# Kernel tuning notes

Measured on AMD Instinct MI355X. Metric: run time of the kernel, lower is better.

## Reference

```python
import jax, jax.numpy as jnp
import numpy as np

BETA = 0.95      # leak
THRESH = 1.0     # snntorch Leaky default threshold
ALPHA = 2.0      # ATan surrogate alpha (atan_with_alpha)
T = 100          # SPIKE_STEPS
D_IN = 65536     # input_dims
HID = 256        # fc1 hidden (hardcoded)
N_OUT = 20       # n_actions(2) * NUM_NEURONS_PER_ACTION(10)


def spike_fn(x):
    # forward of snntorch surrogate.ATan: Heaviside
    return (x > 0.0).astype(x.dtype)


def lif_step(mem, cur):
    # snntorch Leaky, reset_mechanism='subtract':
    # reset computed from previous membrane (detached), then decay+integrate, then fire
    reset = jax.lax.stop_gradient((mem > THRESH).astype(mem.dtype))
    mem_new = BETA * mem + cur - reset * THRESH
    spk = spike_fn(mem_new - THRESH)
    return spk, mem_new


def _run_net(x, W1, b1, W2, b2):
    # x: [T, D_IN]. Precompute all layer-1 currents as one big GEMM, then scan the recurrence.
    cur1_all = x @ W1.T + b1  # [T, HID]

    def step(carry, cur1):
        mem1, mem2 = carry
        spk1, mem1 = lif_step(mem1, cur1)
        cur2 = spk1 @ W2.T + b2  # [n_out]
        spk2, mem2 = lif_step(mem2, cur2)
        return (mem1, mem2), spk2

    init = (jnp.zeros((W1.shape[0],), x.dtype), jnp.zeros((W2.shape[0],), x.dtype))
    (_, mem2_final), spk2_hist = jax.lax.scan(step, init, cur1_all)
    return spk2_hist, mem2_final  # [T, n_out], [n_out]


def setup_inputs() -> dict:
    key = jax.random.key(0)
    ks = jax.random.split(key, 5)
    s = 0.01
    return {
        "poisson_spikes": jax.random.uniform(ks[0], (T, 1, D_IN), dtype=jnp.float32),
        "aW1": jax.random.normal(ks[1], (HID, D_IN), dtype=jnp.float32) * s,
        "ab1": jnp.zeros((HID,), jnp.float32),
        "aW2": jax.random.normal(ks[2], (N_OUT, HID), dtype=jnp.float32) * s,
        "ab2": jnp.zeros((N_OUT,), jnp.float32),
        "cW1": jax.random.normal(ks[3], (HID, D_IN), dtype=jnp.float32) * s,
        "cb1": jnp.zeros((HID,), jnp.float32),
        "cW2": jax.random.normal(ks[4], (1, HID), dtype=jnp.float32) * s,
        "cb2": jnp.zeros((1,), jnp.float32),
    }


def reference(poisson_spikes, aW1, ab1, aW2, ab2, cW1, cb1, cW2, cb2):
    x = poisson_spikes[:, 0, :]  # effective batch of 1 -> [T, D_IN]
    actor_spk_hist, _ = _run_net(x, aW1, ab1, aW2, ab2)        # [T, 20]
    _, critic_mem = _run_net(x, cW1, cb1, cW2, cb2)            # [1]
    spk_sum = actor_spk_hist.sum(axis=0)                       # [20] (sum over timesteps)
    action_vals = jnp.stack([spk_sum[:10].sum(), spk_sum[10:].sum()])
    policy = jax.nn.softmax(action_vals)                       # [2]
    return policy, critic_mem
```

## Files before the change

### kernel.cpp

```cpp
#include <hip/hip_runtime.h>
#include <hip/hip_bf16.h>

#define T_STEPS 100
#define D_IN    65536
#define HID     256
#define HTOT    512
#define BETA    0.95f
#define THRESH  1.0f

typedef __bf16 bf16x8 __attribute__((ext_vector_type(8)));
typedef float  f32x16 __attribute__((ext_vector_type(16)));

__device__ __forceinline__ void gload_lds16(const void* g, void* l) {
    __builtin_amdgcn_global_load_lds(
        (const __attribute__((address_space(1))) void*)g,
        (__attribute__((address_space(3))) void*)l, 16, 0, 0);
}

__global__ __launch_bounds__(256, 2) void k_gemm1(
    const float* __restrict__ aW1,
    const float* __restrict__ cW1,
    const float* __restrict__ x,
    float* __restrict__ P,
    int nsteps)
{
    const int d    = blockIdx.x;
    const int xcd  = d & 7;
    const int sl   = d >> 3;
    const int s    = xcd * 16 + (sl & 15);
    const int ht   = sl >> 4;

    const int tid  = threadIdx.x;
    const int lane = tid & 63;
    const int l31  = lane & 31;
    const int h5   = lane >> 5;
    const int wv   = tid >> 6;
    const int wt   = (wv & 1) * 64;
    const int wh   = (wv >> 1) * 64;

    __shared__ __align__(16) char smem[2][32768];

    const float* Wbase = (ht < 2) ? (aW1 + (size_t)ht * 128 * D_IN)
                                  : (cW1 + (size_t)(ht - 2) * 128 * D_IN);

    const float* xsrc[4];
    const float* wsrc[4];
#pragma unroll
    for (int o = 0; o < 4; o++) {
        const int idx = o * 256 + tid;
        const int row = idx >> 3, g = idx & 7;
        const int xrow = (row < T_STEPS) ? row : (T_STEPS - 1);
        xsrc[o] = x     + (size_t)xrow * D_IN + (g ^ (row & 7)) * 4;
        wsrc[o] = Wbase + (size_t)row  * D_IN + (g ^ (row & 7)) * 4;
    }
    const int gk0 = s * nsteps;

    f32x16 acc00, acc01, acc10, acc11;
#pragma unroll
    for (int i = 0; i < 16; i++) {
        acc00[i] = 0.f; acc01[i] = 0.f; acc10[i] = 0.f; acc11[i] = 0.f;
    }

#define STAGE(i) do {                                                         \
    char* b_ = smem[(i) & 1];                                                 \
    const int kc_ = (gk0 + (i)) * 32;                                         \
    _Pragma("unroll")                                                         \
    for (int o = 0; o < 4; o++) {                                             \
        const int g_ = o * 256 + tid;                                         \
        gload_lds16(xsrc[o] + kc_, b_ + g_ * 16);                             \
    }                                                                         \
    _Pragma("unroll")                                                         \
    for (int o = 0; o < 4; o++) {                                             \
        const int g_ = o * 256 + tid;                                         \
        gload_lds16(wsrc[o] + kc_, b_ + 16384 + g_ * 16);                     \
    }                                                                         \
} while (0)

#define CVT8(dsth, dstm, va, vb) do {                                         \
    float f_[8] = {va.x, va.y, va.z, va.w, vb.x, vb.y, vb.z, vb.w};           \
    _Pragma("unroll")                                                         \
    for (int e = 0; e < 8; e++) {                                             \
        __bf16 h = (__bf16)f_[e];                                             \
        dsth[e] = h; dstm[e] = (__bf16)(f_[e] - (float)h);                    \
    }                                                                         \
} while (0)

#define COMPUTE(i) do {                                                       \
    const char* b_ = smem[(i) & 1];                                           \
    _Pragma("unroll")                                                         \
    for (int s16 = 0; s16 < 2; s16++) {                                       \
        const int slot_ = s16 * 2 + h5;                                       \
        const int gb    = slot_ * 2;                                          \
            \
        const int r0 = wt + l31, r1 = r0 + 32;                                \
        const char* xr0_ = b_ + r0 * 128;                                     \
        const char* xr1_ = b_ + r1 * 128;                                     \
        float4 xa0 = *(const float4*)(xr0_ + ((gb ^ (r0 & 7)) * 16));         \
        float4 xb0 = *(const float4*)(xr0_ + (((gb + 1) ^ (r0 & 7)) * 16));   \
        float4 xa1 = *(const float4*)(xr1_ + ((gb ^ (r1 & 7)) * 16));         \
        float4 xb1 = *(const float4*)(xr1_ + (((gb + 1) ^ (r1 & 7)) * 16));   \
        bf16x8 a0h, a0m, a1h, a1m;                                            \
        CVT8(a0h, a0m, xa0, xb0);                                             \
        CVT8(a1h, a1m, xa1, xb1);                                             \
                      \
        const int hrA = wh + l31, hrB = hrA + 32;                             \
        const char* wrA_ = b_ + 16384 + hrA * 128;                            \
        const char* wrB_ = b_ + 16384 + hrB * 128;                            \
        float4 waA = *(const float4*)(wrA_ + ((gb ^ (hrA & 7)) * 16));        \
        float4 wbA = *(const float4*)(wrA_ + (((gb + 1) ^ (hrA & 7)) * 16));  \
        float4 waB = *(const float4*)(wrB_ + ((gb ^ (hrB & 7)) * 16));        \
        float4 wbB = *(const float4*)(wrB_ + (((gb + 1) ^ (hrB & 7)) * 16));  \
        bf16x8 bhA, bmA, bhB, bmB;                                            \
        CVT8(bhA, bmA, waA, wbA);                                             \
        CVT8(bhB, bmB, waB, wbB);                                             \
        acc00 = __builtin_amdgcn_mfma_f32_32x32x16_bf16(a0m, bhA, acc00, 0,0,0); \
        acc00 = __builtin_amdgcn_mfma_f32_32x32x16_bf16(a0h, bmA, acc00, 0,0,0); \
        acc00 = __builtin_amdgcn_mfma_f32_32x32x16_bf16(a0h, bhA, acc00, 0,0,0); \
        acc01 = __builtin_amdgcn_mfma_f32_32x32x16_bf16(a0m, bhB, acc01, 0,0,0); \
        acc01 = __builtin_amdgcn_mfma_f32_32x32x16_bf16(a0h, bmB, acc01, 0,0,0); \
        acc01 = __builtin_amdgcn_mfma_f32_32x32x16_bf16(a0h, bhB, acc01, 0,0,0); \
        acc10 = __builtin_amdgcn_mfma_f32_32x32x16_bf16(a1m, bhA, acc10, 0,0,0); \
        acc10 = __builtin_amdgcn_mfma_f32_32x32x16_bf16(a1h, bmA, acc10, 0,0,0); \
        acc10 = __builtin_amdgcn_mfma_f32_32x32x16_bf16(a1h, bhA, acc10, 0,0,0); \
        acc11 = __builtin_amdgcn_mfma_f32_32x32x16_bf16(a1m, bhB, acc11, 0,0,0); \
        acc11 = __builtin_amdgcn_mfma_f32_32x32x16_bf16(a1h, bmB, acc11, 0,0,0); \
        acc11 = __builtin_amdgcn_mfma_f32_32x32x16_bf16(a1h, bhB, acc11, 0,0,0); \
    }                                                                         \
} while (0)

    STAGE(0);
    STAGE(1);
    for (int i = 0; i < nsteps; i++) {
        if (i + 1 < nsteps) asm volatile("s_waitcnt vmcnt(8)" ::: "memory");
        else                asm volatile("s_waitcnt vmcnt(0)" ::: "memory");
        __builtin_amdgcn_s_barrier();
        __builtin_amdgcn_sched_barrier(0);
        COMPUTE(i);
        __builtin_amdgcn_s_barrier();
        __builtin_amdgcn_sched_barrier(0);
        if (i + 2 < nsteps) STAGE(i + 2);
    }
#undef STAGE
#undef CVT8
#undef COMPUTE

    const int rbase = 4 * h5;
    float* Pb = P + (size_t)s * T_STEPS * HTOT;
    const int hA = ht * 128 + wh + l31;
    const int hB = hA + 32;
#pragma unroll
    for (int reg = 0; reg < 16; reg++) {
        const int row = (reg & 3) + rbase + 8 * (reg >> 2);
        const int t0  = wt + row;
        const int t1  = wt + 32 + row;
        if (t0 < T_STEPS) {
            Pb[(size_t)t0 * HTOT + hA] = acc00[reg];
            Pb[(size_t)t0 * HTOT + hB] = acc01[reg];
        }
        if (t1 < T_STEPS) {
            Pb[(size_t)t1 * HTOT + hA] = acc10[reg];
            Pb[(size_t)t1 * HTOT + hB] = acc11[reg];
        }
    }
}

__global__ __launch_bounds__(256) void k_reduce(
    const float* __restrict__ P,
    const float* __restrict__ ab1, const float* __restrict__ cb1,
    float* __restrict__ cur1, int NS)
{
    int g4 = blockIdx.x * 256 + threadIdx.x;
    int g  = g4 * 4;
    int h0 = g & (HTOT - 1);
    float4 sum;
    sum.x = (h0 + 0 < HID) ? ab1[h0 + 0] : cb1[h0 + 0 - HID];
    sum.y = (h0 + 1 < HID) ? ab1[h0 + 1] : cb1[h0 + 1 - HID];
    sum.z = (h0 + 2 < HID) ? ab1[h0 + 2] : cb1[h0 + 2 - HID];
    sum.w = (h0 + 3 < HID) ? ab1[h0 + 3] : cb1[h0 + 3 - HID];
    for (int ss = 0; ss < NS; ss++) {
        float4 v = *(const float4*)(P + (size_t)ss * T_STEPS * HTOT + g);
        sum.x += v.x; sum.y += v.y; sum.z += v.z; sum.w += v.w;
    }
    *(float4*)(cur1 + g) = sum;
}

__global__ __launch_bounds__(64) void k_lif1(
    const float* __restrict__ cur1,
    unsigned long long* __restrict__ bitsws,
    float* __restrict__ wsa)
{
    const int b    = blockIdx.x;
    const int lane = threadIdx.x;
    const int n    = b * 64 + lane;

    float mem = 0.f;
    for (int tb = 0; tb < T_STEPS; tb += 10) {
        float c[10];
#pragma unroll
        for (int i = 0; i < 10; i++) c[i] = cur1[(size_t)(tb + i) * HTOT + n];
#pragma unroll
        for (int i = 0; i < 10; i++) {
            float reset = (mem > THRESH) ? THRESH : 0.f;
            mem = BETA * mem + c[i] - reset;
            unsigned long long m = __ballot(mem > THRESH);
            if (lane == 0) bitsws[(size_t)(tb + i) * 8 + b] = m;
        }
    }
    if (b == 0 && lane == 0) { wsa[0] = 0.f; wsa[1] = 0.f; }
}

__global__ __launch_bounds__(128) void k_gemm2(
    const unsigned long long* __restrict__ bitsws,
    const float* __restrict__ aW2, const float* __restrict__ ab2,
    const float* __restrict__ cW2, const float* __restrict__ cb2,
    float* __restrict__ wsa, float* __restrict__ out)
{
    const int j   = blockIdx.x;
    const int tid = threadIdx.x;

    __shared__ float W[256];
    __shared__ float c2[T_STEPS];

    const float* Wsrc = (j < 20) ? (aW2 + j * 256) : cW2;
    for (int i = tid; i < 256; i += 128) W[i] = Wsrc[i];
    const float bias  = (j < 20) ? ab2[j] : cb2[0];
    const int   wbase = (j < 20) ? 0 : 4;
    __syncthreads();

    const int t = tid;
    if (t < T_STEPS) {
        unsigned long long m0 = bitsws[(size_t)t * 8 + wbase + 0];
        unsigned long long m1 = bitsws[(size_t)t * 8 + wbase + 1];
        unsigned long long m2 = bitsws[(size_t)t * 8 + wbase + 2];
        unsigned long long m3 = bitsws[(size_t)t * 8 + wbase + 3];
        float acc = bias;
#pragma unroll
        for (int bitp = 0; bitp < 64; bitp++) {
            acc += ((m0 >> bitp) & 1ULL) ? W[bitp]       : 0.f;
            acc += ((m1 >> bitp) & 1ULL) ? W[64 + bitp]  : 0.f;
            acc += ((m2 >> bitp) & 1ULL) ? W[128 + bitp] : 0.f;
            acc += ((m3 >> bitp) & 1ULL) ? W[192 + bitp] : 0.f;
        }
        c2[t] = acc;
    }
    __syncthreads();

    if (tid == 0) {
        float mem = 0.f, spk = 0.f;
        for (int tt = 0; tt < T_STEPS; tt++) {
            float reset = (mem > THRESH) ? THRESH : 0.f;
            mem = BETA * mem + c2[tt] - reset;
            spk += (mem > THRESH) ? 1.f : 0.f;
        }
        if (j < 10)       atomicAdd(&wsa[0], spk);
        else if (j < 20)  atomicAdd(&wsa[1], spk);
        else              out[2] = mem;
    }
}

__global__ __launch_bounds__(64) void k_final(
    const float* __restrict__ wsa, float* __restrict__ out)
{
    if (threadIdx.x == 0) {
        float a0 = wsa[0], a1 = wsa[1];
        float mx = fmaxf(a0, a1);
        float e0 = expf(a0 - mx), e1 = expf(a1 - mx);
        float inv = 1.f / (e0 + e1);
        out[0] = e0 * inv;
        out[1] = e1 * inv;
    }
}

extern "C" void kernel_launch(void* const* d_in, const int* in_sizes, int n_in,
                              void* d_out, int out_size, void* d_ws, size_t ws_size,
                              hipStream_t stream) {
    const float* x   = (const float*)d_in[0];
    const float* aW1 = (const float*)d_in[1];
    const float* ab1 = (const float*)d_in[2];
    const float* aW2 = (const float*)d_in[3];
    const float* ab2 = (const float*)d_in[4];
    const float* cW1 = (const float*)d_in[5];
    const float* cb1 = (const float*)d_in[6];
    const float* cW2 = (const float*)d_in[7];
    const float* cb2 = (const float*)d_in[8];
    float* out = (float*)d_out;

    const int NS = 128;
    const int nsteps = (D_IN / NS) / 32;

    float* P    = (float*)d_ws;
    float* cur1 = P + (size_t)NS * T_STEPS * HTOT;
    unsigned long long* bitsws =
        (unsigned long long*)(cur1 + T_STEPS * HTOT);
    float* wsa = (float*)(bitsws + T_STEPS * 8);

    k_gemm1 <<<512, 256, 0, stream>>>(aW1, cW1, x, P, nsteps);
    k_reduce<<<(T_STEPS * HTOT / 4) / 256, 256, 0, stream>>>(P, ab1, cb1, cur1, NS);
    k_lif1  <<<8, 64, 0, stream>>>(cur1, bitsws, wsa);
    k_gemm2 <<<21, 128, 0, stream>>>(bitsws, aW2, ab2, cW2, cb2, wsa, out);
    k_final <<<1, 64, 0, stream>>>(wsa, out);
}
```

Before: 92.77 us.

## Split x and W LDS staging: single-buffer 64-wide W tiles, double-buffer x

Separates the staging of x and W into LDS. x keeps its double buffer of 32-column chunks, while W now goes into a single 64-column buffer with a 16-way swizzle that is reloaded every other step. This issues fewer, larger W loads and changes the vmcnt wait depth. It assumes nsteps is even. With W single-buffered, its load is no longer overlapped a full step ahead, which may expose latency.

Result: slower. 96.84 us (+4.4%).

```diff
diff --git a/kernel.cpp b/kernel.cpp
--- a/kernel.cpp
+++ b/kernel.cpp
@@ -38,22 +38,28 @@
     const int wt   = (wv & 1) * 64;
     const int wh   = (wv >> 1) * 64;
 
-    __shared__ __align__(16) char smem[2][32768];
+    __shared__ __align__(16) char smem[65536];
 
     const float* Wbase = (ht < 2) ? (aW1 + (size_t)ht * 128 * D_IN)
                                   : (cW1 + (size_t)(ht - 2) * 128 * D_IN);
 
     const float* xsrc[4];
-    const float* wsrc[4];
 #pragma unroll
     for (int o = 0; o < 4; o++) {
         const int idx = o * 256 + tid;
         const int row = idx >> 3, g = idx & 7;
         const int xrow = (row < T_STEPS) ? row : (T_STEPS - 1);
-        xsrc[o] = x     + (size_t)xrow * D_IN + (g ^ (row & 7)) * 4;
-        wsrc[o] = Wbase + (size_t)row  * D_IN + (g ^ (row & 7)) * 4;
+        xsrc[o] = x + (size_t)xrow * D_IN + (g ^ (row & 7)) * 4;
+    }
+    const float* wsrc[8];
+#pragma unroll
+    for (int o = 0; o < 8; o++) {
+        const int idx = o * 256 + tid;
+        const int row = idx >> 4, g = idx & 15;
+        wsrc[o] = Wbase + (size_t)row * D_IN + ((g ^ (row & 15)) * 4);
     }
     const int gk0 = s * nsteps;
+    const int gw0 = s * (nsteps >> 1);
 
     f32x16 acc00, acc01, acc10, acc11;
 #pragma unroll
@@ -61,18 +67,22 @@
         acc00[i] = 0.f; acc01[i] = 0.f; acc10[i] = 0.f; acc11[i] = 0.f;
     }
 
-#define STAGE(i) do {                                                         \
-    char* b_ = smem[(i) & 1];                                                 \
+#define XSTAGE(i) do {                                                        \
+    char* b_ = smem + ((i) & 1) * 16384;                                      \
     const int kc_ = (gk0 + (i)) * 32;                                         \
     _Pragma("unroll")                                                         \
     for (int o = 0; o < 4; o++) {                                             \
         const int g_ = o * 256 + tid;                                         \
         gload_lds16(xsrc[o] + kc_, b_ + g_ * 16);                             \
     }                                                                         \
+} while (0)
+
+#define WSTAGE(w) do {                                                        \
+    const int kc_ = (gw0 + (w)) * 64;                                         \
     _Pragma("unroll")                                                         \
-    for (int o = 0; o < 4; o++) {                                             \
+    for (int o = 0; o < 8; o++) {                                             \
         const int g_ = o * 256 + tid;                                         \
-        gload_lds16(wsrc[o] + kc_, b_ + 16384 + g_ * 16);                     \
+        gload_lds16(wsrc[o] + kc_, smem + 32768 + g_ * 16);                   \
     }                                                                         \
 } while (0)
 
@@ -86,30 +96,32 @@
 } while (0)
 
 #define COMPUTE(i) do {                                                       \
-    const char* b_ = smem[(i) & 1];                                           \
+    const char* b_ = smem + ((i) & 1) * 16384;                                \
+    const char* wb_ = smem + 32768;                                           \
+    const int khalf_ = (i) & 1;                                               \
     _Pragma("unroll")                                                         \
     for (int s16 = 0; s16 < 2; s16++) {                                       \
-        const int slot_ = s16 * 2 + h5;                                       \
-        const int gb    = slot_ * 2;                                          \
-            \
+        const int gba = s16 * 4 + h5 * 2;           \
+        const int gbw = khalf_ * 8 + gba;          \
+                                         \
         const int r0 = wt + l31, r1 = r0 + 32;                                \
         const char* xr0_ = b_ + r0 * 128;                                     \
         const char* xr1_ = b_ + r1 * 128;                                     \
-        float4 xa0 = *(const float4*)(xr0_ + ((gb ^ (r0 & 7)) * 16));         \
-        float4 xb0 = *(const float4*)(xr0_ + (((gb + 1) ^ (r0 & 7)) * 16));   \
-        float4 xa1 = *(const float4*)(xr1_ + ((gb ^ (r1 & 7)) * 16));         \
-        float4 xb1 = *(const float4*)(xr1_ + (((gb + 1) ^ (r1 & 7)) * 16));   \
+        float4 xa0 = *(const float4*)(xr0_ + ((gba ^ (r0 & 7)) * 16));        \
+        float4 xb0 = *(const float4*)(xr0_ + (((gba + 1) ^ (r0 & 7)) * 16));  \
+        float4 xa1 = *(const float4*)(xr1_ + ((gba ^ (r1 & 7)) * 16));        \
+        float4 xb1 = *(const float4*)(xr1_ + (((gba + 1) ^ (r1 & 7)) * 16));  \
         bf16x8 a0h, a0m, a1h, a1m;                                            \
         CVT8(a0h, a0m, xa0, xb0);                                             \
         CVT8(a1h, a1m, xa1, xb1);                                             \
-                      \
+                  \
         const int hrA = wh + l31, hrB = hrA + 32;                             \
-        const char* wrA_ = b_ + 16384 + hrA * 128;                            \
-        const char* wrB_ = b_ + 16384 + hrB * 128;                            \
-        float4 waA = *(const float4*)(wrA_ + ((gb ^ (hrA & 7)) * 16));        \
-        float4 wbA = *(const float4*)(wrA_ + (((gb + 1) ^ (hrA & 7)) * 16));  \
-        float4 waB = *(const float4*)(wrB_ + ((gb ^ (hrB & 7)) * 16));        \
-        float4 wbB = *(const float4*)(wrB_ + (((gb + 1) ^ (hrB & 7)) * 16));  \
+        const char* wrA_ = wb_ + hrA * 256;                                   \
+        const char* wrB_ = wb_ + hrB * 256;                                   \
+        float4 waA = *(const float4*)(wrA_ + ((gbw ^ (hrA & 15)) * 16));      \
+        float4 wbA = *(const float4*)(wrA_ + (((gbw + 1) ^ (hrA & 15)) * 16));\
+        float4 waB = *(const float4*)(wrB_ + ((gbw ^ (hrB & 15)) * 16));      \
+        float4 wbB = *(const float4*)(wrB_ + (((gbw + 1) ^ (hrB & 15)) * 16));\
         bf16x8 bhA, bmA, bhB, bmB;                                            \
         CVT8(bhA, bmA, waA, wbA);                                             \
         CVT8(bhB, bmB, waB, wbB);                                             \
@@ -128,19 +140,25 @@
     }                                                                         \
 } while (0)
 
-    STAGE(0);
-    STAGE(1);
+    WSTAGE(0);
+    XSTAGE(0);
+    XSTAGE(1);
     for (int i = 0; i < nsteps; i++) {
-        if (i + 1 < nsteps) asm volatile("s_waitcnt vmcnt(8)" ::: "memory");
+        if (i + 1 < nsteps) asm volatile("s_waitcnt vmcnt(4)" ::: "memory");
         else                asm volatile("s_waitcnt vmcnt(0)" ::: "memory");
         __builtin_amdgcn_s_barrier();
         __builtin_amdgcn_sched_barrier(0);
         COMPUTE(i);
         __builtin_amdgcn_s_barrier();
         __builtin_amdgcn_sched_barrier(0);
-        if (i + 2 < nsteps) STAGE(i + 2);
-    }
-#undef STAGE
+        if (i & 1) {
+            const int w = (i + 1) >> 1;
+            if (w < (nsteps >> 1)) WSTAGE(w);
+        }
+        if (i + 2 < nsteps) XSTAGE(i + 2);
+    }
+#undef XSTAGE
+#undef WSTAGE
 #undef CVT8
 #undef COMPUTE
 
```
